# Optimization experiments

Hardware: AMD Instinct MI355X
Metric: run time of the kernel (lower is better)

## Reference

```python
import jax, jax.numpy as jnp
import numpy as np


def _clenshaw_curtiss(nlat):
    # equiangular nodes including poles: theta_k = pi*k/(n-1)
    n = nlat
    theta = np.pi * np.arange(n) / (n - 1)
    jmax = (n - 1) // 2
    j = np.arange(1, jmax + 1)
    b = np.where(2 * j == (n - 1), 1.0, 2.0)
    # v_k = 1 - sum_j b_j/(4j^2-1) cos(2 j theta_k)
    v = 1.0 - (b / (4.0 * j**2 - 1.0)) @ np.cos(2.0 * np.outer(j, theta))
    w = (2.0 / (n - 1)) * v
    w[0] *= 0.5
    w[-1] *= 0.5
    return theta, w  # quadrature on [-1,1], sum(w)=2


def _precompute_legpoly(mmax, lmax, theta, csphase=True):
    # orthonormal associated Legendre P_l^m(cos theta), shape (mmax, lmax, nlat)
    nlat = theta.shape[0]
    x = np.cos(theta)
    s = np.sin(theta)
    pct = np.zeros((mmax, lmax, nlat), dtype=np.float64)
    pmm = np.full(nlat, np.sqrt(1.0 / (4.0 * np.pi)))  # P_0^0
    sign = -1.0 if csphase else 1.0
    for m in range(mmax):
        if m > 0:
            pmm = sign * np.sqrt((2.0 * m + 1.0) / (2.0 * m)) * s * pmm
        if m < lmax:
            pct[m, m] = pmm
        if m + 1 < lmax:
            p_prev = pmm
            p = np.sqrt(2.0 * m + 3.0) * x * pmm
            pct[m, m + 1] = p
            for l in range(m + 2, lmax):
                a = np.sqrt((4.0 * l * l - 1.0) / (l * l - m * m))
                b = np.sqrt(((l - 1.0) ** 2 - m * m) / (4.0 * (l - 1.0) ** 2 - 1.0))
                p_new = a * (x * p - b * p_prev)
                pct[m, l] = p_new
                p_prev, p = p, p_new
    return pct


def _make_weights(nlat, lmax, mmax):
    theta, w = _clenshaw_curtiss(nlat)
    pct = _precompute_legpoly(mmax, lmax, theta, csphase=True)
    # fold quadrature weights in: 'mlk,k->mlk'
    return (pct * w[None, None, :]).astype(np.float32)


NLAT, NLON, LMAX, MMAX = 361, 720, 361, 361


def setup_inputs() -> dict:
    key = jax.random.key(0)
    x = jax.random.normal(key, (1, 256, NLAT, NLON), dtype=jnp.float32)
    weights = jnp.asarray(_make_weights(NLAT, LMAX, MMAX))  # (mmax, lmax, nlat)
    return {"x": x, "weights": weights}


def reference(x, weights):
    nlon = x.shape[-1]
    mmax = weights.shape[0]
    # rfft along longitude, 'forward' norm (divide by nlon), truncate to mmax, scale 2*pi
    xf = (2.0 * jnp.pi / nlon) * jnp.fft.rfft(x, axis=-1)[..., :mmax]  # (B,C,nlat,mmax)
    xr = jnp.swapaxes(xf.real, -1, -2)  # (B,C,mmax,nlat)
    xi = jnp.swapaxes(xf.imag, -1, -2)
    out_re = jnp.einsum('bcmk,mlk->bclm', xr, weights)  # (B,C,lmax,mmax)
    out_im = jnp.einsum('bcmk,mlk->bclm', xi, weights)
    return jax.lax.complex(out_re, out_im)
```

## Files before the change

### kernel.cpp

```cpp
#include <hip/hip_runtime.h>
#include <math.h>

#define TWO_PI 6.283185307179586f


typedef __attribute__((ext_vector_type(8))) short bf16x8;
typedef __attribute__((ext_vector_type(4))) float f32x4;

__device__ inline unsigned short f2bf(float f) {
    union { float f; unsigned int u; } v; v.f = f;
    unsigned int u = v.u;
    return (unsigned short)((u + 0x7fffu + ((u >> 16) & 1u)) >> 16);
}
__device__ inline float bf2f(unsigned short h) {
    union { unsigned int u; float f; } v; v.u = ((unsigned int)h) << 16;
    return v.f;
}
__device__ inline unsigned int packhl(float v) {
    unsigned short h = f2bf(v);
    unsigned short l = f2bf(v - bf2f(h));
    return (unsigned int)h | ((unsigned int)l << 16);
}
__device__ inline void split2(float a, float b, unsigned int& hh, unsigned int& ll) {
    unsigned short ha = f2bf(a), hb = f2bf(b);
    unsigned short la = f2bf(a - bf2f(ha)), lb = f2bf(b - bf2f(hb));
    hh = (unsigned int)ha | ((unsigned int)hb << 16);
    ll = (unsigned int)la | ((unsigned int)lb << 16);
}
__device__ inline void split2t(float a, float b, unsigned int& hh, unsigned int& ll) {
    union { float f; unsigned int u; } ua, ub, fa, fb, la, lb;
    ua.f = a; ub.f = b;
    hh = (ua.u >> 16) | (ub.u & 0xffff0000u);
    fa.u = ua.u & 0xffff0000u;
    fb.u = ub.u & 0xffff0000u;
    la.f = a - fa.f;
    lb.f = b - fb.f;
    ll = (la.u >> 16) | (lb.u & 0xffff0000u);
}
__device__ inline void gload_lds16(const void* g, void* l) {
    __builtin_amdgcn_global_load_lds(
        (const __attribute__((address_space(1))) unsigned int*)g,
        (__attribute__((address_space(3))) unsigned int*)l, 16, 0, 0);
}
__device__ inline int xcd_work(int bid, int nwg) {
    int q = nwg >> 3, r = nwg & 7;
    int xcd = bid & 7, ord = bid >> 3;
    return (xcd < r ? xcd * (q + 1) : r * (q + 1) + (xcd - r) * q) + ord;
}

__global__ void build_ect(unsigned short* __restrict__ Eh,
                          unsigned short* __restrict__ El) {
    const float sigma = TWO_PI / 720.0f;
    const int total = 384 * 192;
    for (int i = blockIdx.x * blockDim.x + threadIdx.x; i < total;
         i += gridDim.x * blockDim.x) {
        int row = i / 192, n = i % 192;
        int g = row / 192 ? 1 : 0;
        int mg = row - g * 192;
        int m = 2 * mg + g;
        float v = 0.f;
        if (m <= 360 && n <= 180) {
            int r = (n * m) % 720;
            v = sigma * cosf((float)r * (TWO_PI / 720.0f));
            if (n == 180) v *= 0.5f;
        }
        unsigned short h = f2bf(v);
        Eh[i] = h;
        El[i] = f2bf(v - bf2f(h));
    }
}

__global__ __launch_bounds__(256, 4) void s1_mfma(
    const float* __restrict__ x, const unsigned short* __restrict__ Eh,
    const unsigned short* __restrict__ El, unsigned int* __restrict__ xrp,
    const int Q) {
    __shared__ short Ah[2][4][64][8], Al[2][4][64][8];
    __shared__ short Bt[2][2][4][96][8];

    const int work = xcd_work(blockIdx.x, gridDim.x);
    const int q0 = (work >> 2) * 64;
    const int tt = work & 3;
    const int grp = tt >> 1;
    const int m0g = (tt & 1) * 96;
    const int t = threadIdx.x;
    const int lane = t & 63, wv = t >> 6;
    const int lr = lane & 15, lk = lane >> 4;
    const int wq = wv;

    const int ar = t >> 2, akc = t & 3;
    const int aq = q0 + ar;
    const float* arow = x + (size_t)aq * 720;
    const bool aqv = (aq < Q);

    const unsigned short* bsrc[3];
#pragma unroll
    for (int i = 0; i < 3; ++i) {
        int id = t + i * 256;
        int tab = id / 384, rem = id % 384;
        int kc = rem / 96, r = rem % 96;
        bsrc[i] = (tab ? El : Eh) + (size_t)(grp * 192 + m0g + r) * 192 + kc * 8;
    }

    f32x4 acc[6];
#pragma unroll
    for (int nj = 0; nj < 6; ++nj)
#pragma unroll
        for (int r = 0; r < 4; ++r) acc[nj][r] = 0.f;

    float4 f1a, f1b, f2a, f2b, r1a, r1b, r2a, r2b;

#define S1_LOADA(K0)                                                       \
    {                                                                      \
        int kg = (K0) + akc * 8;                                           \
        f1a = make_float4(0.f, 0.f, 0.f, 0.f);                             \
        f1b = f1a; f2a = f1a; f2b = f1a;                                   \
        r1a = f1a; r1b = f1a; r2a = f1a; r2b = f1a;                        \
        if (aqv) {                                                         \
            f1a = *(const float4*)(arow + kg);                             \
            f1b = *(const float4*)(arow + kg + 4);                         \
            f2a = *(const float4*)(arow + 360 + kg);                       \
            f2b = *(const float4*)(arow + 364 + kg);                       \
            r2a = *(const float4*)(arow + 353 - kg);                       \
            r2b = *(const float4*)(arow + 357 - kg);                       \
            if (kg >= 8) {                                                 \
                r1a = *(const float4*)(arow + 713 - kg);                   \
                r1b = *(const float4*)(arow + 717 - kg);                   \
            } else {                                                       \
                float tm[8];                                               \
                _Pragma("unroll") for (int i = 0; i < 8; ++i)              \
                    tm[i] = (7 - i >= 1) ? arow[713 + i] : 0.f;            \
                r1a = make_float4(tm[0], tm[1], tm[2], tm[3]);             \
                r1b = make_float4(tm[4], tm[5], tm[6], tm[7]);             \
            }                                                              \
        }                                                                  \
    }
#define S1_WRITEA(NB, K0)                                                  \
    {                                                                      \
        int kg = (K0) + akc * 8;                                           \
        float b0 = f1a.x + r1b.w, b1 = f1a.y + r1b.z;                      \
        float b2 = f1a.z + r1b.y, b3 = f1a.w + r1b.x;                      \
        float b4 = f1b.x + r1a.w, b5 = f1b.y + r1a.z;                      \
        float b6 = f1b.z + r1a.y, b7 = f1b.w + r1a.x;                      \
        float p0 = r2b.w + ((kg == 0) ? 0.f : f2a.x);                      \
        float p1 = r2b.z + f2a.y, p2 = r2b.y + f2a.z, p3 = r2b.x + f2a.w;  \
        float p4 = r2a.w + f2b.x, p5 = r2a.z + f2b.y;                      \
        float p6 = r2a.y + f2b.z, p7 = r2a.x + f2b.w;                      \
        float s = grp ? -1.f : 1.f;                                        \
        float y0 = b0 + s * p0, y1 = b1 + s * p1;                          \
        float y2 = b2 + s * p2, y3 = b3 + s * p3;                          \
        float y4 = b4 + s * p4, y5 = b5 + s * p5;                          \
        float y6 = b6 + s * p6, y7 = b7 + s * p7;                          \
        if (kg > 172) {                                                    \
            if (kg + 0 > 180) y0 = 0.f;                                    \
            if (kg + 1 > 180) y1 = 0.f;                                    \
            if (kg + 2 > 180) y2 = 0.f;                                    \
            if (kg + 3 > 180) y3 = 0.f;                                    \
            if (kg + 4 > 180) y4 = 0.f;                                    \
            if (kg + 5 > 180) y5 = 0.f;                                    \
            if (kg + 6 > 180) y6 = 0.f;                                    \
            if (kg + 7 > 180) y7 = 0.f;                                    \
        }                                                                  \
        unsigned int h0, h1, h2, h3, l0, l1, l2, l3;                      \
        split2t(y0, y1, h0, l0);                                          \
        split2t(y2, y3, h1, l1);                                          \
        split2t(y4, y5, h2, l2);                                          \
        split2t(y6, y7, h3, l3);                                          \
        *(uint4*)&Ah[NB][akc][ar][0] = make_uint4(h0, h1, h2, h3);        \
        *(uint4*)&Al[NB][akc][ar][0] = make_uint4(l0, l1, l2, l3);        \
    }
#define S1_COPYB(NB, K0)                                                  \
    {                                                                     \
        char* bb = (char*)&Bt[NB][0][0][0][0];                            \
        _Pragma("unroll") for (int i = 0; i < 3; ++i) {                   \
            gload_lds16(bsrc[i] + (K0), bb + (t + i * 256) * 16);         \
        }                                                                 \
    }

    S1_COPYB(0, 0);
    S1_LOADA(0);
    S1_WRITEA(0, 0);
    __syncthreads();
    int cur = 0;
    const int NIT = 6;
    for (int it = 0; it < NIT; ++it) {
        const int nb = cur ^ 1;
        if (it + 1 < NIT) {
            S1_COPYB(nb, (it + 1) * 32);
            S1_LOADA((it + 1) * 32);
        }
        bf16x8 ah = *(const bf16x8*)&Ah[cur][lk][wq * 16 + lr][0];
        bf16x8 al = *(const bf16x8*)&Al[cur][lk][wq * 16 + lr][0];
#pragma unroll
        for (int nj = 0; nj < 6; ++nj) {
            bf16x8 bh = *(const bf16x8*)&Bt[cur][0][lk][nj * 16 + lr][0];
            bf16x8 bl = *(const bf16x8*)&Bt[cur][1][lk][nj * 16 + lr][0];
            acc[nj] = __builtin_amdgcn_mfma_f32_16x16x32_bf16(ah, bh, acc[nj], 0, 0, 0);
            acc[nj] = __builtin_amdgcn_mfma_f32_16x16x32_bf16(ah, bl, acc[nj], 0, 0, 0);
            acc[nj] = __builtin_amdgcn_mfma_f32_16x16x32_bf16(al, bh, acc[nj], 0, 0, 0);
        }
        if (it + 1 < NIT) {
            S1_WRITEA(nb, (it + 1) * 32);
            __syncthreads();
            cur = nb;
        }
    }

#pragma unroll
    for (int nj = 0; nj < 6; ++nj) {
        int mg = m0g + nj * 16 + lr;
        int m = 2 * mg + grp;
        if (m >= 361) continue;
        size_t base = (size_t)m * Q;
#pragma unroll
        for (int reg = 0; reg < 4; ++reg) {
            int q = q0 + wq * 16 + lk * 4 + reg;
            if (q < Q) xrp[base + q] = packhl(acc[nj][reg]);
        }
    }
}

__global__ __launch_bounds__(256, 4) void s2_mfma(
    const unsigned int* __restrict__ xrp, const float* __restrict__ W,
    float* __restrict__ stg, const int CH) {
    __shared__ short Ah[128][40], Al[128][40];
    __shared__ short Bh[64][40], Bl[64][40];

    const int work = xcd_work(blockIdx.x, gridDim.x);
    const int m = work / 12;
    const int rem = work % 12;
    const int half = rem / 6, lt = rem % 6;
    const int l0 = lt * 64;
    if (l0 + 63 < m) return;
    const int bcbase = half * 128;
    if (bcbase >= CH) return;
    const int Q = CH * 361;
    const int t = threadIdx.x;
    const int lane = t & 63, wv = t >> 6;
    const int lr = lane & 15, lk = lane >> 4;
    const int wbc = wv >> 1, wl = wv & 1;

    const unsigned int* Am = xrp + (size_t)m * Q;
    const float* Wm = W + (size_t)m * 130321;

    f32x4 acc[4][2];
#pragma unroll
    for (int fi = 0; fi < 4; ++fi)
#pragma unroll
        for (int ni = 0; ni < 2; ++ni)
#pragma unroll
            for (int r = 0; r < 4; ++r) acc[fi][ni][r] = 0.f;

    unsigned int pa0[8], pa1[8];
    float wva[4], wvb[4];

#define S2_LOADR(K0)                                                          \
    {                                                                         \
        _Pragma("unroll") for (int i = 0; i < 8; ++i) {                       \
            int id = t + i * 256;                                             \
            int r = id >> 4, kp = id & 15;                                    \
            int bc = bcbase + r, kg = (K0) + kp * 2;                          \
            unsigned int p0 = 0, p1 = 0;                                      \
            if (bc < CH) {                                                    \
                size_t base = (size_t)bc * 361;                               \
                if (kg < 361) p0 = Am[base + kg];                             \
                if (kg + 1 < 361) p1 = Am[base + kg + 1];                     \
            }                                                                 \
            pa0[i] = p0; pa1[i] = p1;                                         \
        }                                                                     \
        _Pragma("unroll") for (int i = 0; i < 4; ++i) {                       \
            int id = t + i * 256;                                             \
            int r = id >> 4, kp = id & 15;                                    \
            int l = l0 + r, kg = (K0) + kp * 2;                               \
            float va = 0.f, vb = 0.f;                                         \
            if (l < 361) {                                                    \
                size_t base = (size_t)l * 361;                                \
                if (kg < 361) va = Wm[base + kg];                             \
                if (kg + 1 < 361) vb = Wm[base + kg + 1];                     \
            }                                                                 \
            wva[i] = va; wvb[i] = vb;                                         \
        }                                                                     \
    }
#define S2_WRITES()                                                           \
    {                                                                         \
        _Pragma("unroll") for (int i = 0; i < 8; ++i) {                       \
            int id = t + i * 256;                                             \
            int r = id >> 4, kp = id & 15;                                    \
            *(unsigned int*)&Ah[r][kp * 2] =                                  \
                (pa0[i] & 0xffffu) | (pa1[i] << 16);                          \
            *(unsigned int*)&Al[r][kp * 2] =                                  \
                (pa0[i] >> 16) | (pa1[i] & 0xffff0000u);                      \
        }                                                                     \
        _Pragma("unroll") for (int i = 0; i < 4; ++i) {                       \
            int id = t + i * 256;                                             \
            int r = id >> 4, kp = id & 15;                                    \
            unsigned int hh, ll;                                              \
            split2(wva[i], wvb[i], hh, ll);                                   \
            *(unsigned int*)&Bh[r][kp * 2] = hh;                              \
            *(unsigned int*)&Bl[r][kp * 2] = ll;                              \
        }                                                                     \
    }

    S2_LOADR(0);
    S2_WRITES();
    __syncthreads();
    for (int it = 0; it < 12; ++it) {
        if (it + 1 < 12) S2_LOADR((it + 1) * 32);
#pragma unroll
        for (int fi = 0; fi < 4; ++fi) {
            bf16x8 ah = *(const bf16x8*)&Ah[wbc * 64 + fi * 16 + lr][lk * 8];
            bf16x8 al = *(const bf16x8*)&Al[wbc * 64 + fi * 16 + lr][lk * 8];
#pragma unroll
            for (int ni = 0; ni < 2; ++ni) {
                bf16x8 bh = *(const bf16x8*)&Bh[wl * 32 + ni * 16 + lr][lk * 8];
                bf16x8 bl = *(const bf16x8*)&Bl[wl * 32 + ni * 16 + lr][lk * 8];
                acc[fi][ni] = __builtin_amdgcn_mfma_f32_16x16x32_bf16(ah, bh, acc[fi][ni], 0, 0, 0);
                acc[fi][ni] = __builtin_amdgcn_mfma_f32_16x16x32_bf16(ah, bl, acc[fi][ni], 0, 0, 0);
                acc[fi][ni] = __builtin_amdgcn_mfma_f32_16x16x32_bf16(al, bh, acc[fi][ni], 0, 0, 0);
            }
        }
        __syncthreads();
        if (it + 1 < 12) {
            S2_WRITES();
            __syncthreads();
        }
    }

#pragma unroll
    for (int fi = 0; fi < 4; ++fi) {
#pragma unroll
        for (int ni = 0; ni < 2; ++ni) {
            int l = l0 + wl * 32 + ni * 16 + lr;
#pragma unroll
            for (int reg = 0; reg < 4; ++reg) {
                int bc = bcbase + wbc * 64 + fi * 16 + lk * 4 + reg;
                if (bc < CH && l < 361)
                    stg[((size_t)m * CH + bc) * 361 + l] = acc[fi][ni][reg];
            }
        }
    }
}

__global__ __launch_bounds__(256) void transpose_out(const float* __restrict__ stg,
                                                     float* __restrict__ out,
                                                     const int c0, const int CH) {
    __shared__ float tile[32][33];
    const int Q = CH * 361;
    const int m0 = blockIdx.y * 32, q0 = blockIdx.x * 32;
    const int tx = threadIdx.x & 31, ty = threadIdx.x >> 5;
    for (int i = ty; i < 32; i += 8) {
        int mm = m0 + i, q = q0 + tx;
        float v = 0.f;
        if (mm < 361 && q < Q) {
            int l = q % 361;
            if ((l | 63) >= mm) v = stg[(size_t)mm * Q + q];
        }
        tile[i][tx] = v;
    }
    __syncthreads();
    for (int i = ty; i < 32; i += 8) {
        int q = q0 + i, mm = m0 + tx;
        if (mm < 361 && q < Q)
            out[((size_t)c0 * 361 + q) * 361 + mm] = tile[tx][i];
    }
}

extern "C" void kernel_launch(void* const* d_in, const int* in_sizes, int n_in,
                              void* d_out, int out_size, void* d_ws, size_t ws_size,
                              hipStream_t stream) {
    (void)out_size;
    const float* x = (const float*)d_in[0];
    const float* W = (const float*)d_in[1];
    if (n_in >= 2 && (in_sizes[0] == 47045881 || in_sizes[1] == 66539520)) {
        x = (const float*)d_in[1];
        W = (const float*)d_in[0];
    }
    float* out = (float*)d_out;

    const size_t offEh = 0;
    const size_t offEl = 147456;
    const size_t offData = 294912;

    const int cands[6] = {256, 128, 64, 32, 16, 8};
    int CH = 0;
    for (int i = 0; i < 6; ++i) {
        size_t need = offData + 2ull * cands[i] * 130321ull * 4ull;
        if (need <= ws_size) { CH = cands[i]; break; }
    }
    if (!CH) return;

    unsigned short* Eh = (unsigned short*)((char*)d_ws + offEh);
    unsigned short* El = (unsigned short*)((char*)d_ws + offEl);
    unsigned int* xrp = (unsigned int*)((char*)d_ws + offData);
    float* stg = (float*)((char*)d_ws + offData + (size_t)CH * 130321ull * 4ull);

    build_ect<<<256, 256, 0, stream>>>(Eh, El);

    const int Q = CH * 361;
    const int qt = (Q + 63) / 64;
    for (int c0 = 0; c0 < 256; c0 += CH) {
        s1_mfma<<<qt * 4, 256, 0, stream>>>(
            x + (size_t)c0 * 361 * 720, Eh, El, xrp, Q);
        s2_mfma<<<361 * 12, 256, 0, stream>>>(xrp, W, stg, CH);
        transpose_out<<<dim3((Q + 31) / 32, 12), 256, 0, stream>>>(stg, out, c0, CH);
    }
}
```

Baseline: 561.6 us.

## Exploit Legendre parity symmetry to halve the latitude contraction in stage two

```diff
diff --git a/kernel.cpp b/kernel.cpp
--- a/kernel.cpp
+++ b/kernel.cpp
@@ -20,6 +20,9 @@
     unsigned short h = f2bf(v);
     unsigned short l = f2bf(v - bf2f(h));
     return (unsigned int)h | ((unsigned int)l << 16);
+}
+__device__ inline float unpackhl(unsigned int p) {
+    return bf2f((unsigned short)(p & 0xffffu)) + bf2f((unsigned short)(p >> 16));
 }
 __device__ inline void split2(float a, float b, unsigned int& hh, unsigned int& ll) {
     unsigned short ha = f2bf(a), hb = f2bf(b);
@@ -219,27 +222,59 @@
     }
 }
 
+__global__ __launch_bounds__(256) void fold_uv(const unsigned int* __restrict__ xrp,
+                                               unsigned int* __restrict__ up,
+                                               unsigned int* __restrict__ vp,
+                                               const int CH) {
+    const int total = 361 * CH * 192;
+    const int Q = CH * 361;
+    for (int i = blockIdx.x * blockDim.x + threadIdx.x; i < total;
+         i += gridDim.x * blockDim.x) {
+        int m = i / (CH * 192);
+        int rem = i - m * (CH * 192);
+        int bc = rem / 192;
+        int k = rem - bc * 192;
+        float u = 0.f, v = 0.f;
+        if (k <= 180) {
+            size_t base = (size_t)m * Q + (size_t)bc * 361;
+            float x1 = unpackhl(xrp[base + k]);
+            if (k < 180) {
+                float x2 = unpackhl(xrp[base + 360 - k]);
+                u = x1 + x2;
+                v = x1 - x2;
+            } else {
+                u = x1;
+                v = x1;
+            }
+        }
+        up[i] = packhl(u);
+        vp[i] = packhl(v);
+    }
+}
+
 __global__ __launch_bounds__(256, 4) void s2_mfma(
-    const unsigned int* __restrict__ xrp, const float* __restrict__ W,
-    float* __restrict__ stg, const int CH) {
+    const unsigned int* __restrict__ up, const unsigned int* __restrict__ vp,
+    const float* __restrict__ W, float* __restrict__ stg, const int CH) {
     __shared__ short Ah[128][40], Al[128][40];
     __shared__ short Bh[64][40], Bl[64][40];
 
     const int work = xcd_work(blockIdx.x, gridDim.x);
     const int m = work / 12;
     const int rem = work % 12;
-    const int half = rem / 6, lt = rem % 6;
-    const int l0 = lt * 64;
-    if (l0 + 63 < m) return;
+    const int half = rem / 6;
+    const int r2 = rem % 6;
+    const int g = r2 / 3, lgt = r2 % 3;
+    const int lg0 = lgt * 64;
+    const int par = (g + m) & 1;
+    if (2 * (lg0 + 63) + par < m) return;
     const int bcbase = half * 128;
     if (bcbase >= CH) return;
-    const int Q = CH * 361;
     const int t = threadIdx.x;
     const int lane = t & 63, wv = t >> 6;
     const int lr = lane & 15, lk = lane >> 4;
     const int wbc = wv >> 1, wl = wv & 1;
 
-    const unsigned int* Am = xrp + (size_t)m * Q;
+    const unsigned int* Am = (g ? vp : up) + (size_t)m * CH * 192;
     const float* Wm = W + (size_t)m * 130321;
 
     f32x4 acc[4][2];
@@ -261,21 +296,21 @@
             int bc = bcbase + r, kg = (K0) + kp * 2;                          \
             unsigned int p0 = 0, p1 = 0;                                      \
             if (bc < CH) {                                                    \
-                size_t base = (size_t)bc * 361;                               \
-                if (kg < 361) p0 = Am[base + kg];                             \
-                if (kg + 1 < 361) p1 = Am[base + kg + 1];                     \
+                size_t base = (size_t)bc * 192;                               \
+                p0 = Am[base + kg];                                           \
+                p1 = Am[base + kg + 1];                                       \
             }                                                                 \
             pa0[i] = p0; pa1[i] = p1;                                         \
         }                                                                     \
         _Pragma("unroll") for (int i = 0; i < 4; ++i) {                       \
             int id = t + i * 256;                                             \
             int r = id >> 4, kp = id & 15;                                    \
-            int l = l0 + r, kg = (K0) + kp * 2;                               \
+            int l = 2 * (lg0 + r) + par, kg = (K0) + kp * 2;                  \
             float va = 0.f, vb = 0.f;                                         \
             if (l < 361) {                                                    \
                 size_t base = (size_t)l * 361;                                \
-                if (kg < 361) va = Wm[base + kg];                             \
-                if (kg + 1 < 361) vb = Wm[base + kg + 1];                     \
+                if (kg <= 180) va = Wm[base + kg];                            \
+                if (kg + 1 <= 180) vb = Wm[base + kg + 1];                    \
             }                                                                 \
             wva[i] = va; wvb[i] = vb;                                         \
         }                                                                     \
@@ -303,8 +338,8 @@
     S2_LOADR(0);
     S2_WRITES();
     __syncthreads();
-    for (int it = 0; it < 12; ++it) {
-        if (it + 1 < 12) S2_LOADR((it + 1) * 32);
+    for (int it = 0; it < 6; ++it) {
+        if (it + 1 < 6) S2_LOADR((it + 1) * 32);
 #pragma unroll
         for (int fi = 0; fi < 4; ++fi) {
             bf16x8 ah = *(const bf16x8*)&Ah[wbc * 64 + fi * 16 + lr][lk * 8];
@@ -319,7 +354,7 @@
             }
         }
         __syncthreads();
-        if (it + 1 < 12) {
+        if (it + 1 < 6) {
             S2_WRITES();
             __syncthreads();
         }
@@ -329,7 +364,7 @@
     for (int fi = 0; fi < 4; ++fi) {
 #pragma unroll
         for (int ni = 0; ni < 2; ++ni) {
-            int l = l0 + wl * 32 + ni * 16 + lr;
+            int l = 2 * (lg0 + wl * 32 + ni * 16 + lr) + par;
 #pragma unroll
             for (int reg = 0; reg < 4; ++reg) {
                 int bc = bcbase + wbc * 64 + fi * 16 + lk * 4 + reg;
@@ -352,7 +387,9 @@
         float v = 0.f;
         if (mm < 361 && q < Q) {
             int l = q % 361;
-            if ((l | 63) >= mm) v = stg[(size_t)mm * Q + q];
+            int par = l & 1;
+            int lg = l >> 1;
+            if (2 * (lg | 63) + par >= mm) v = stg[(size_t)mm * Q + q];
         }
         tile[i][tx] = v;
     }
@@ -383,7 +420,7 @@
     const int cands[6] = {256, 128, 64, 32, 16, 8};
     int CH = 0;
     for (int i = 0; i < 6; ++i) {
-        size_t need = offData + 2ull * cands[i] * 130321ull * 4ull;
+        size_t need = offData + (size_t)cands[i] * (130321ull * 2 + 69312ull * 2) * 4;
         if (need <= ws_size) { CH = cands[i]; break; }
     }
     if (!CH) return;
@@ -391,7 +428,9 @@
     unsigned short* Eh = (unsigned short*)((char*)d_ws + offEh);
     unsigned short* El = (unsigned short*)((char*)d_ws + offEl);
     unsigned int* xrp = (unsigned int*)((char*)d_ws + offData);
-    float* stg = (float*)((char*)d_ws + offData + (size_t)CH * 130321ull * 4ull);
+    unsigned int* up = xrp + (size_t)CH * 130321;
+    unsigned int* vp = up + (size_t)CH * 69312;
+    float* stg = (float*)(vp + (size_t)CH * 69312);
 
     build_ect<<<256, 256, 0, stream>>>(Eh, El);
 
@@ -400,7 +439,8 @@
     for (int c0 = 0; c0 < 256; c0 += CH) {
         s1_mfma<<<qt * 4, 256, 0, stream>>>(
             x + (size_t)c0 * 361 * 720, Eh, El, xrp, Q);
-        s2_mfma<<<361 * 12, 256, 0, stream>>>(xrp, W, stg, CH);
+        fold_uv<<<8192, 256, 0, stream>>>(xrp, up, vp, CH);
+        s2_mfma<<<361 * 12, 256, 0, stream>>>(up, vp, W, stg, CH);
         transpose_out<<<dim3((Q + 31) / 32, 12), 256, 0, stream>>>(stg, out, c0, CH);
     }
 }
```

After: 542.8 us, median of 2. -3.4%, faster.

## Exploit Legendre equatorial symmetry to halve the contraction length in the Legendre stage

Applied to the files above, without the earlier changes.

```diff
diff --git a/kernel.cpp b/kernel.cpp
--- a/kernel.cpp
+++ b/kernel.cpp
@@ -20,6 +20,9 @@
     unsigned short h = f2bf(v);
     unsigned short l = f2bf(v - bf2f(h));
     return (unsigned int)h | ((unsigned int)l << 16);
+}
+__device__ inline float unpackhl(unsigned int p) {
+    return bf2f((unsigned short)(p & 0xffffu)) + bf2f((unsigned short)(p >> 16));
 }
 __device__ inline void split2(float a, float b, unsigned int& hh, unsigned int& ll) {
     unsigned short ha = f2bf(a), hb = f2bf(b);
@@ -228,9 +231,12 @@
     const int work = xcd_work(blockIdx.x, gridDim.x);
     const int m = work / 12;
     const int rem = work % 12;
-    const int half = rem / 6, lt = rem % 6;
-    const int l0 = lt * 64;
-    if (l0 + 63 < m) return;
+    const int half = rem / 6;
+    const int r2 = rem % 6;
+    const int g = r2 / 3, lgt = r2 % 3;
+    const int lg0 = lgt * 64;
+    const int par = (g + m) & 1;
+    if (2 * (lg0 + 63) + par < m) return;
     const int bcbase = half * 128;
     if (bcbase >= CH) return;
     const int Q = CH * 361;
@@ -241,6 +247,7 @@
 
     const unsigned int* Am = xrp + (size_t)m * Q;
     const float* Wm = W + (size_t)m * 130321;
+    const float sgn = g ? -1.f : 1.f;
 
     f32x4 acc[4][2];
 #pragma unroll
@@ -250,7 +257,7 @@
 #pragma unroll
             for (int r = 0; r < 4; ++r) acc[fi][ni][r] = 0.f;
 
-    unsigned int pa0[8], pa1[8];
+    unsigned int paf0[8], paf1[8], par0[8], par1[8];
     float wva[4], wvb[4];
 
 #define S2_LOADR(K0)                                                          \
@@ -259,23 +266,29 @@
             int id = t + i * 256;                                             \
             int r = id >> 4, kp = id & 15;                                    \
             int bc = bcbase + r, kg = (K0) + kp * 2;                          \
-            unsigned int p0 = 0, p1 = 0;                                      \
+            unsigned int f0 = 0, f1 = 0, v0 = 0, v1 = 0;                      \
             if (bc < CH) {                                                    \
                 size_t base = (size_t)bc * 361;                               \
-                if (kg < 361) p0 = Am[base + kg];                             \
-                if (kg + 1 < 361) p1 = Am[base + kg + 1];                     \
+                if (kg <= 180) {                                              \
+                    f0 = Am[base + kg];                                       \
+                    if (kg < 180) v0 = Am[base + 360 - kg];                   \
+                }                                                             \
+                if (kg + 1 <= 180) {                                          \
+                    f1 = Am[base + kg + 1];                                   \
+                    if (kg + 1 < 180) v1 = Am[base + 359 - kg];               \
+                }                                                             \
             }                                                                 \
-            pa0[i] = p0; pa1[i] = p1;                                         \
+            paf0[i] = f0; paf1[i] = f1; par0[i] = v0; par1[i] = v1;           \
         }                                                                     \
         _Pragma("unroll") for (int i = 0; i < 4; ++i) {                       \
             int id = t + i * 256;                                             \
             int r = id >> 4, kp = id & 15;                                    \
-            int l = l0 + r, kg = (K0) + kp * 2;                               \
+            int l = 2 * (lg0 + r) + par, kg = (K0) + kp * 2;                  \
             float va = 0.f, vb = 0.f;                                         \
             if (l < 361) {                                                    \
                 size_t base = (size_t)l * 361;                                \
-                if (kg < 361) va = Wm[base + kg];                             \
-                if (kg + 1 < 361) vb = Wm[base + kg + 1];                     \
+                if (kg <= 180) va = Wm[base + kg];                            \
+                if (kg + 1 <= 180) vb = Wm[base + kg + 1];                    \
             }                                                                 \
             wva[i] = va; wvb[i] = vb;                                         \
         }                                                                     \
@@ -285,10 +298,12 @@
         _Pragma("unroll") for (int i = 0; i < 8; ++i) {                       \
             int id = t + i * 256;                                             \
             int r = id >> 4, kp = id & 15;                                    \
-            *(unsigned int*)&Ah[r][kp * 2] =                                  \
-                (pa0[i] & 0xffffu) | (pa1[i] << 16);                          \
-            *(unsigned int*)&Al[r][kp * 2] =                                  \
-                (pa0[i] >> 16) | (pa1[i] & 0xffff0000u);                      \
+            float u0 = unpackhl(paf0[i]) + sgn * unpackhl(par0[i]);           \
+            float u1 = unpackhl(paf1[i]) + sgn * unpackhl(par1[i]);           \
+            unsigned int hh, ll;                                              \
+            split2(u0, u1, hh, ll);                                           \
+            *(unsigned int*)&Ah[r][kp * 2] = hh;                              \
+            *(unsigned int*)&Al[r][kp * 2] = ll;                              \
         }                                                                     \
         _Pragma("unroll") for (int i = 0; i < 4; ++i) {                       \
             int id = t + i * 256;                                             \
@@ -303,8 +318,8 @@
     S2_LOADR(0);
     S2_WRITES();
     __syncthreads();
-    for (int it = 0; it < 12; ++it) {
-        if (it + 1 < 12) S2_LOADR((it + 1) * 32);
+    for (int it = 0; it < 6; ++it) {
+        if (it + 1 < 6) S2_LOADR((it + 1) * 32);
 #pragma unroll
         for (int fi = 0; fi < 4; ++fi) {
             bf16x8 ah = *(const bf16x8*)&Ah[wbc * 64 + fi * 16 + lr][lk * 8];
@@ -319,7 +334,7 @@
             }
         }
         __syncthreads();
-        if (it + 1 < 12) {
+        if (it + 1 < 6) {
             S2_WRITES();
             __syncthreads();
         }
@@ -329,7 +344,7 @@
     for (int fi = 0; fi < 4; ++fi) {
 #pragma unroll
         for (int ni = 0; ni < 2; ++ni) {
-            int l = l0 + wl * 32 + ni * 16 + lr;
+            int l = 2 * (lg0 + wl * 32 + ni * 16 + lr) + par;
 #pragma unroll
             for (int reg = 0; reg < 4; ++reg) {
                 int bc = bcbase + wbc * 64 + fi * 16 + lk * 4 + reg;
@@ -352,7 +367,9 @@
         float v = 0.f;
         if (mm < 361 && q < Q) {
             int l = q % 361;
-            if ((l | 63) >= mm) v = stg[(size_t)mm * Q + q];
+            int par = l & 1;
+            int lg = l >> 1;
+            if (2 * (lg | 63) + par >= mm) v = stg[(size_t)mm * Q + q];
         }
         tile[i][tx] = v;
     }
@@ -383,7 +400,7 @@
     const int cands[6] = {256, 128, 64, 32, 16, 8};
     int CH = 0;
     for (int i = 0; i < 6; ++i) {
-        size_t need = offData + 2ull * cands[i] * 130321ull * 4ull;
+        size_t need = offData + (size_t)cands[i] * (130321ull * 2) * 4;
         if (need <= ws_size) { CH = cands[i]; break; }
     }
     if (!CH) return;
@@ -391,7 +408,7 @@
     unsigned short* Eh = (unsigned short*)((char*)d_ws + offEh);
     unsigned short* El = (unsigned short*)((char*)d_ws + offEl);
     unsigned int* xrp = (unsigned int*)((char*)d_ws + offData);
-    float* stg = (float*)((char*)d_ws + offData + (size_t)CH * 130321ull * 4ull);
+    float* stg = (float*)(xrp + (size_t)CH * 130321);
 
     build_ect<<<256, 256, 0, stream>>>(Eh, El);
 
```

Result: slower. 743.6 us (+32.4%).
